# Optimization experiments

Measured on AMD Instinct MI355X. Metric: run time of the kernel, lower is better.

The kernel has to match this reference:

```python
import jax, jax.numpy as jnp
import numpy as np

CODEBOOK_SIZE = 1024
NUM_GROUPS = 8
CODES_PER_GROUP = CODEBOOK_SIZE // NUM_GROUPS
COMMITMENT_COST = 0.25


def setup_inputs() -> dict:
    key = jax.random.key(0)
    k1, k2, k3 = jax.random.split(key, 3)
    B, C, H, W = 32, 256, 32, 32
    z = jax.random.normal(k1, (B, C, H, W), dtype=jnp.float32)
    # matches nn.Embedding init: uniform(-1/n_e, 1/n_e)
    emb_weight = jax.random.uniform(
        k2, (CODEBOOK_SIZE, C), dtype=jnp.float32,
        minval=-1.0 / CODEBOOK_SIZE, maxval=1.0 / CODEBOOK_SIZE)
    # proj initialized near identity (nn.init.eye_), perturbed so it is non-trivial
    proj_weight = jnp.eye(C, dtype=jnp.float32) + 0.01 * jax.random.normal(
        k3, (C, C), dtype=jnp.float32)
    return {"z": z, "emb_weight": emb_weight, "proj_weight": proj_weight}


def reference(z, emb_weight, proj_weight):
    # z: [B, C, H, W] -> [B, H, W, C]
    B, C, H, W = z.shape
    zc = jnp.transpose(z, (0, 2, 3, 1))          # bhwc
    zf = zc.reshape(-1, C)                        # [N, C], N = B*H*W

    # codebook = embedding_proj(embedding.weight) = emb @ proj.T
    codebook = emb_weight @ proj_weight.T         # [n_e, C]

    # squared L2 distances: [N, n_e]
    d = (jnp.sum(zf * zf, axis=1, keepdims=True)
         + jnp.sum(codebook * codebook, axis=1)
         - 2.0 * (zf @ codebook.T))

    # group-restricted mask: token group depends on width position
    pos_groups = (jnp.arange(W) * NUM_GROUPS) // W          # [W]
    token_groups = jnp.tile(pos_groups, B * H)              # [N]
    code_groups = jnp.arange(CODEBOOK_SIZE) // CODES_PER_GROUP  # [n_e]
    valid = token_groups[:, None] == code_groups[None, :]   # [N, n_e]
    d = jnp.where(valid, d, jnp.inf)

    idx = jnp.argmin(d, axis=1)                   # [N]
    zq = codebook[idx].reshape(zc.shape)          # [B, H, W, C]

    commitment_loss = COMMITMENT_COST * jnp.mean(
        (jax.lax.stop_gradient(zq) - zc) ** 2)
    codebook_loss = jnp.mean((zq - jax.lax.stop_gradient(zc)) ** 2)
    loss = commitment_loss + codebook_loss

    # straight-through estimator
    zq_ste = zc + jax.lax.stop_gradient(zq - zc)
    zq_out = jnp.transpose(zq_ste, (0, 3, 1, 2))  # [B, C, H, W]

    return (zq_out, loss, commitment_loss, codebook_loss,
            idx.reshape(B, H, W))
```

## Files before the change

### kernel.cpp

```cpp
#include <hip/hip_runtime.h>

#define CODEBOOK 1024
#define NGROUPS  8
#define CPG      128
#define Bn 32
#define Cn 256
#define Hn 32
#define Wn 32

#define ZQ_OFF   0
#define LOSS_OFF (Bn*Cn*Hn*Wn)
#define IDX_OFF  (LOSS_OFF + 3)

__global__ __launch_bounds__(256) void transpose_proj(const float* __restrict__ proj,
                                                      float* __restrict__ projT,
                                                      double* __restrict__ lacc) {
    if (blockIdx.x == 0 && threadIdx.x == 0) lacc[0] = 0.0;
    int k = blockIdx.x;
    int j = threadIdx.x;
    projT[(size_t)k * Cn + j] = proj[(size_t)j * Cn + k];
}

__global__ __launch_bounds__(256) void codebook_kernel(const float* __restrict__ emb,
                                                       const float* __restrict__ projT,
                                                       float* __restrict__ cb) {
    __shared__ float emb8[8][Cn];
    const int t  = threadIdx.x;
    const int i0 = blockIdx.x * 8;
#pragma unroll
    for (int m = 0; m < 8; ++m) {
        int id = t + m * 256;
        int ci = id >> 8, k = id & 255;
        emb8[ci][k] = emb[(size_t)(i0 + ci) * Cn + k];
    }
    __syncthreads();
    float acc[8] = {0.f,0.f,0.f,0.f,0.f,0.f,0.f,0.f};
    for (int k = 0; k < Cn; ++k) {
        float pj = projT[(size_t)k * Cn + t];
#pragma unroll
        for (int ci = 0; ci < 8; ++ci)
            acc[ci] = __builtin_fmaf(emb8[ci][k], pj, acc[ci]);
    }
#pragma unroll
    for (int ci = 0; ci < 8; ++ci)
        cb[(size_t)(i0 + ci) * Cn + t] = acc[ci];
}

__global__ __launch_bounds__(64) void norm_kernel(const float* __restrict__ cb,
                                                  float* __restrict__ norms) {
    int i = blockIdx.x, l = threadIdx.x;
    float4 v = *(const float4*)(cb + (size_t)i * Cn + l * 4);
    float s = v.x*v.x + v.y*v.y + v.z*v.z + v.w*v.w;
#pragma unroll
    for (int off = 32; off > 0; off >>= 1) s += __shfl_down(s, off);
    if (l == 0) norms[i] = s;
}

__global__ __launch_bounds__(256) void vq_main(const float* __restrict__ z,
                                               const float* __restrict__ cb,
                                               const float* __restrict__ norms,
                                               float* __restrict__ out,
                                               double* __restrict__ lacc) {
    __shared__ float ztile[64][64];
    __shared__ float cbt[128][64];
    __shared__ float zfin[64];
    __shared__ float red_d[64][16];
    __shared__ int   red_c[64][16];
    __shared__ int   bestidx[64];

    const int t   = threadIdx.x;
    const int bid = blockIdx.x;
    const int r   = bid & 7;
    const int q   = bid >> 3;
    const int g   = q & 7;
    const int s   = ((q >> 3) << 3) | r;
    const int ht  = s & 1;
    const int b   = s >> 1;
    const int h0  = ht * 16;
    const int w0  = g * 4;

    const float* zb  = z  + (size_t)b * (Cn * Hn * Wn);
    const float* cbg = cb + (size_t)g * CPG * Cn;

    const int tok0  = (t & 15) * 4;
    const int code0 = (t >> 4) * 8;

    float acc[4][8];
#pragma unroll
    for (int rr2 = 0; rr2 < 4; ++rr2)
#pragma unroll
        for (int c = 0; c < 8; ++c) acc[rr2][c] = 0.f;

    float zr[16];
#pragma unroll
    for (int p = 0; p < 16; ++p) zr[p] = 0.f;

    for (int kc = 0; kc < 4; ++kc) {
        const int k0 = kc * 64;
#pragma unroll
        for (int m = 0; m < 4; ++m) {
            int id = t + m * 256;
            int kk = id >> 4, i = id & 15;
            float4 v = *(const float4*)(zb + (size_t)(k0 + kk) * (Hn * Wn)
                                        + (h0 + i) * Wn + w0);
            *(float4*)&ztile[kk][i * 4] = v;
        }
#pragma unroll
        for (int m = 0; m < 8; ++m) {
            int id = t + m * 256;
            int ci = id >> 4, kq = id & 15;
            float4 v = *(const float4*)(cbg + (size_t)ci * Cn + k0 + kq * 4);
            ((float4*)&cbt[ci][0])[kq ^ (ci >> 3)] = v;
        }
        __syncthreads();

        if (t < 64) {
#pragma clang fp contract(off)
            {
                const int base8 = (kc >> 1) * 8;
                for (int kk = 0; kk < 64; ++kk) {
                    float v  = ztile[kk][t];
                    float sq = v * v;
                    zr[base8 + (kk & 7)] += sq;
                }
            }
        }

        for (int kb = 0; kb < 16; ++kb) {
            const int kk = kb * 4;
            float4 zt[4];
#pragma unroll
            for (int u = 0; u < 4; ++u)
                zt[u] = *(const float4*)&ztile[kk + u][tok0];
            float4 cf[8];
#pragma unroll
            for (int c = 0; c < 8; ++c)
                cf[c] = ((const float4*)&cbt[code0 + c][0])[kb ^ ((code0 + c) >> 3)];
#pragma unroll
            for (int u = 0; u < 4; ++u) {
                const float zu[4] = {
                    zt[u].x, zt[u].y, zt[u].z, zt[u].w };
                const float cu[8] = {
                    ((const float*)&cf[0])[u], ((const float*)&cf[1])[u],
                    ((const float*)&cf[2])[u], ((const float*)&cf[3])[u],
                    ((const float*)&cf[4])[u], ((const float*)&cf[5])[u],
                    ((const float*)&cf[6])[u], ((const float*)&cf[7])[u] };
#pragma unroll
                for (int rr3 = 0; rr3 < 4; ++rr3)
#pragma unroll
                    for (int c = 0; c < 8; ++c)
                        acc[rr3][c] = __builtin_fmaf(zu[rr3], cu[c], acc[rr3][c]);
            }
        }
        __syncthreads();
    }

    if (t < 64) {
#pragma clang fp contract(off)
        {
            float zh0 = ((zr[0] + zr[1]) + (zr[2] + zr[3]))
                      + ((zr[4] + zr[5]) + (zr[6] + zr[7]));
            float zh1 = ((zr[8] + zr[9]) + (zr[10] + zr[11]))
                      + ((zr[12] + zr[13]) + (zr[14] + zr[15]));
            zfin[t] = zh0 + zh1;
        }
    }
    __syncthreads();

    float nv[8];
    *(float4*)&nv[0] = *(const float4*)(norms + g * CPG + code0);
    *(float4*)&nv[4] = *(const float4*)(norms + g * CPG + code0 + 4);
#pragma unroll
    for (int rr4 = 0; rr4 < 4; ++rr4) {
        float zv = zfin[tok0 + rr4];
        float bd = __builtin_inff();
        int   bc = 0;
#pragma unroll
        for (int c = 0; c < 8; ++c) {
            float ss = zv + nv[c];
            float d  = ss - 2.0f * acc[rr4][c];
            if (d < bd) { bd = d; bc = code0 + c; }
        }
        red_d[tok0 + rr4][t >> 4] = bd;
        red_c[tok0 + rr4][t >> 4] = bc;
    }
    __syncthreads();

    if (t < 64) {
        float bd = red_d[t][0];
        int   bc = red_c[t][0];
        for (int p = 1; p < 16; ++p) {
            float d = red_d[t][p];
            if (d < bd) { bd = d; bc = red_c[t][p]; }
        }
        int gidx = g * CPG + bc;
        bestidx[t] = gidx;
        int h = h0 + (t >> 2), w = w0 + (t & 3);
        out[IDX_OFF + b * (Hn * Wn) + h * Wn + w] = (float)gidx;
    }
    __syncthreads();

    float lsum = 0.f;
    const size_t zbase = (size_t)b * (Cn * Hn * Wn);
#pragma unroll
    for (int m = 0; m < 16; ++m) {
        int id = t + m * 256;
        int c = id >> 4, i = id & 15;
        size_t off = zbase + (size_t)c * (Hn * Wn) + (h0 + i) * Wn + w0;
        float4 zv = *(const float4*)(z + off);
        float q0 = cb[(size_t)bestidx[i * 4 + 0] * Cn + c];
        float q1 = cb[(size_t)bestidx[i * 4 + 1] * Cn + c];
        float q2 = cb[(size_t)bestidx[i * 4 + 2] * Cn + c];
        float q3 = cb[(size_t)bestidx[i * 4 + 3] * Cn + c];
        float4 o; o.x = q0; o.y = q1; o.z = q2; o.w = q3;
        *(float4*)(out + ZQ_OFF + off) = o;
        float d0 = q0 - zv.x, d1 = q1 - zv.y, d2 = q2 - zv.z, d3 = q3 - zv.w;
        lsum = __builtin_fmaf(d0, d0, lsum);
        lsum = __builtin_fmaf(d1, d1, lsum);
        lsum = __builtin_fmaf(d2, d2, lsum);
        lsum = __builtin_fmaf(d3, d3, lsum);
    }
    __syncthreads();
    float* rr = &red_d[0][0];
    rr[t] = lsum;
    __syncthreads();
    for (int s2 = 128; s2 > 0; s2 >>= 1) {
        if (t < s2) rr[t] += rr[t + s2];
        __syncthreads();
    }
    if (t == 0) atomicAdd(lacc, (double)rr[0]);
}

__global__ void finalize(const double* __restrict__ lacc, float* __restrict__ out) {
    float M    = (float)(lacc[0] / (double)(Bn * Cn * Hn * Wn));
    float comm = 0.25f * M;
    out[LOSS_OFF + 0] = comm + M;
    out[LOSS_OFF + 1] = comm;
    out[LOSS_OFF + 2] = M;
}

extern "C" void kernel_launch(void* const* d_in, const int* in_sizes, int n_in,
                              void* d_out, int out_size, void* d_ws, size_t ws_size,
                              hipStream_t stream) {
    (void)in_sizes; (void)n_in; (void)out_size; (void)ws_size;
    const float* z    = (const float*)d_in[0];
    const float* emb  = (const float*)d_in[1];
    const float* proj = (const float*)d_in[2];
    float* out = (float*)d_out;

    char*   ws    = (char*)d_ws;
    float*  projT = (float*)ws;
    float*  cb    = (float*)(ws + 262144);
    float*  norms = (float*)(ws + 262144 + 1048576);
    double* lacc  = (double*)(ws + 262144 + 1048576 + 4096);

    transpose_proj <<<Cn,        256, 0, stream>>>(proj, projT, lacc);
    codebook_kernel<<<CODEBOOK/8,256, 0, stream>>>(emb, projT, cb);
    norm_kernel    <<<CODEBOOK,   64, 0, stream>>>(cb, norms);
    vq_main        <<<Bn*2*NGROUPS,256,0, stream>>>(z, cb, norms, out, lacc);
    finalize       <<<1, 1, 0, stream>>>(lacc, out);
}
```

Measured before the change: 175.7 us.

## Fuse codebook, transpose and norm kernels; prefetch tiles; fold finalize into vq_main

```diff
diff --git a/kernel.cpp b/kernel.cpp
--- a/kernel.cpp
+++ b/kernel.cpp
@@ -12,55 +12,72 @@
 #define LOSS_OFF (Bn*Cn*Hn*Wn)
 #define IDX_OFF  (LOSS_OFF + 3)
 
-__global__ __launch_bounds__(256) void transpose_proj(const float* __restrict__ proj,
-                                                      float* __restrict__ projT,
-                                                      double* __restrict__ lacc) {
-    if (blockIdx.x == 0 && threadIdx.x == 0) lacc[0] = 0.0;
-    int k = blockIdx.x;
-    int j = threadIdx.x;
-    projT[(size_t)k * Cn + j] = proj[(size_t)j * Cn + k];
-}
-
-__global__ __launch_bounds__(256) void codebook_kernel(const float* __restrict__ emb,
-                                                       const float* __restrict__ projT,
-                                                       float* __restrict__ cb) {
-    __shared__ float emb8[8][Cn];
+#define KT 32
+__global__ __launch_bounds__(256) void codebook_fused(const float* __restrict__ emb,
+                                                      const float* __restrict__ proj,
+                                                      float* __restrict__ cb,
+                                                      float* __restrict__ norms,
+                                                      double* __restrict__ lacc,
+                                                      int* __restrict__ counter) {
+    __shared__ float emb4[4][Cn];
+    __shared__ float pl[KT][Cn + 1];
     const int t  = threadIdx.x;
-    const int i0 = blockIdx.x * 8;
-#pragma unroll
-    for (int m = 0; m < 8; ++m) {
+    const int i0 = blockIdx.x * 4;
+    if (blockIdx.x == 0 && t == 0) { lacc[0] = 0.0; counter[0] = 0; }
+#pragma unroll
+    for (int m = 0; m < 4; ++m) {
         int id = t + m * 256;
         int ci = id >> 8, k = id & 255;
-        emb8[ci][k] = emb[(size_t)(i0 + ci) * Cn + k];
-    }
-    __syncthreads();
-    float acc[8] = {0.f,0.f,0.f,0.f,0.f,0.f,0.f,0.f};
-    for (int k = 0; k < Cn; ++k) {
-        float pj = projT[(size_t)k * Cn + t];
-#pragma unroll
-        for (int ci = 0; ci < 8; ++ci)
-            acc[ci] = __builtin_fmaf(emb8[ci][k], pj, acc[ci]);
-    }
-#pragma unroll
-    for (int ci = 0; ci < 8; ++ci)
+        emb4[ci][k] = emb[(size_t)(i0 + ci) * Cn + k];
+    }
+    float acc[4] = {0.f, 0.f, 0.f, 0.f};
+    for (int kc = 0; kc < Cn / KT; ++kc) {
+        const int k0 = kc * KT;
+        __syncthreads();
+#pragma unroll
+        for (int m = 0; m < 8; ++m) {
+            int id  = t + m * 256;
+            int row = id >> 3, q = id & 7;
+            float4 v = *(const float4*)(proj + (size_t)row * Cn + k0 + q * 4);
+            pl[q * 4 + 0][row] = v.x;
+            pl[q * 4 + 1][row] = v.y;
+            pl[q * 4 + 2][row] = v.z;
+            pl[q * 4 + 3][row] = v.w;
+        }
+        __syncthreads();
+        for (int kl = 0; kl < KT; ++kl) {
+            float pj = pl[kl][t];
+#pragma unroll
+            for (int ci = 0; ci < 4; ++ci)
+                acc[ci] = __builtin_fmaf(emb4[ci][k0 + kl], pj, acc[ci]);
+        }
+    }
+    __syncthreads();
+    float (*cbrow)[Cn] = (float (*)[Cn])&pl[0][0];
+#pragma unroll
+    for (int ci = 0; ci < 4; ++ci) {
         cb[(size_t)(i0 + ci) * Cn + t] = acc[ci];
-}
-
-__global__ __launch_bounds__(64) void norm_kernel(const float* __restrict__ cb,
-                                                  float* __restrict__ norms) {
-    int i = blockIdx.x, l = threadIdx.x;
-    float4 v = *(const float4*)(cb + (size_t)i * Cn + l * 4);
-    float s = v.x*v.x + v.y*v.y + v.z*v.z + v.w*v.w;
-#pragma unroll
-    for (int off = 32; off > 0; off >>= 1) s += __shfl_down(s, off);
-    if (l == 0) norms[i] = s;
+        cbrow[ci][t] = acc[ci];
+    }
+    __syncthreads();
+    if (t < 64) {
+#pragma unroll
+        for (int ci = 0; ci < 4; ++ci) {
+            float4 v = ((const float4*)&cbrow[ci][0])[t];
+            float s = v.x*v.x + v.y*v.y + v.z*v.z + v.w*v.w;
+#pragma unroll
+            for (int off = 32; off > 0; off >>= 1) s += __shfl_down(s, off);
+            if (t == 0) norms[i0 + ci] = s;
+        }
+    }
 }
 
 __global__ __launch_bounds__(256) void vq_main(const float* __restrict__ z,
                                                const float* __restrict__ cb,
                                                const float* __restrict__ norms,
                                                float* __restrict__ out,
-                                               double* __restrict__ lacc) {
+                                               double* __restrict__ lacc,
+                                               int* __restrict__ counter) {
     __shared__ float ztile[64][64];
     __shared__ float cbt[128][64];
     __shared__ float zfin[64];
@@ -95,24 +112,35 @@
 #pragma unroll
     for (int p = 0; p < 16; ++p) zr[p] = 0.f;
 
+    int z_kk[4], z_i[4], c_ci[8], c_kq[8];
+#pragma unroll
+    for (int m = 0; m < 4; ++m) { int id = t + m * 256; z_kk[m] = id >> 4; z_i[m] = id & 15; }
+#pragma unroll
+    for (int m = 0; m < 8; ++m) { int id = t + m * 256; c_ci[m] = id >> 4; c_kq[m] = id & 15; }
+
+    float4 pz[4], pcb[8];
+    auto issue_loads = [&](int k0) {
+#pragma unroll
+        for (int m = 0; m < 4; ++m)
+            pz[m] = *(const float4*)(zb + (size_t)(k0 + z_kk[m]) * (Hn * Wn)
+                                     + (h0 + z_i[m]) * Wn + w0);
+#pragma unroll
+        for (int m = 0; m < 8; ++m)
+            pcb[m] = *(const float4*)(cbg + (size_t)c_ci[m] * Cn + k0 + c_kq[m] * 4);
+    };
+
+    issue_loads(0);
     for (int kc = 0; kc < 4; ++kc) {
         const int k0 = kc * 64;
-#pragma unroll
-        for (int m = 0; m < 4; ++m) {
-            int id = t + m * 256;
-            int kk = id >> 4, i = id & 15;
-            float4 v = *(const float4*)(zb + (size_t)(k0 + kk) * (Hn * Wn)
-                                        + (h0 + i) * Wn + w0);
-            *(float4*)&ztile[kk][i * 4] = v;
-        }
-#pragma unroll
-        for (int m = 0; m < 8; ++m) {
-            int id = t + m * 256;
-            int ci = id >> 4, kq = id & 15;
-            float4 v = *(const float4*)(cbg + (size_t)ci * Cn + k0 + kq * 4);
-            ((float4*)&cbt[ci][0])[kq ^ (ci >> 3)] = v;
-        }
-        __syncthreads();
+        if (kc) __syncthreads();
+#pragma unroll
+        for (int m = 0; m < 4; ++m)
+            *(float4*)&ztile[z_kk[m]][z_i[m] * 4] = pz[m];
+#pragma unroll
+        for (int m = 0; m < 8; ++m)
+            ((float4*)&cbt[c_ci[m]][0])[c_kq[m] ^ (c_ci[m] >> 3)] = pcb[m];
+        __syncthreads();
+        if (kc < 3) issue_loads(k0 + 64);
 
         if (t < 64) {
 #pragma clang fp contract(off)
@@ -152,7 +180,6 @@
                         acc[rr3][c] = __builtin_fmaf(zu[rr3], cu[c], acc[rr3][c]);
             }
         }
-        __syncthreads();
     }
 
     if (t < 64) {
@@ -228,15 +255,19 @@
         if (t < s2) rr[t] += rr[t + s2];
         __syncthreads();
     }
-    if (t == 0) atomicAdd(lacc, (double)rr[0]);
-}
-
-__global__ void finalize(const double* __restrict__ lacc, float* __restrict__ out) {
-    float M    = (float)(lacc[0] / (double)(Bn * Cn * Hn * Wn));
-    float comm = 0.25f * M;
-    out[LOSS_OFF + 0] = comm + M;
-    out[LOSS_OFF + 1] = comm;
-    out[LOSS_OFF + 2] = M;
+    if (t == 0) {
+        atomicAdd(lacc, (double)rr[0]);
+        __threadfence();
+        int done = atomicAdd(counter, 1);
+        if (done == (int)gridDim.x - 1) {
+            double tot = atomicAdd(lacc, 0.0);
+            float M    = (float)(tot / (double)(Bn * Cn * Hn * Wn));
+            float comm = 0.25f * M;
+            out[LOSS_OFF + 0] = comm + M;
+            out[LOSS_OFF + 1] = comm;
+            out[LOSS_OFF + 2] = M;
+        }
+    }
 }
 
 extern "C" void kernel_launch(void* const* d_in, const int* in_sizes, int n_in,
@@ -248,15 +279,12 @@
     const float* proj = (const float*)d_in[2];
     float* out = (float*)d_out;
 
-    char*   ws    = (char*)d_ws;
-    float*  projT = (float*)ws;
-    float*  cb    = (float*)(ws + 262144);
-    float*  norms = (float*)(ws + 262144 + 1048576);
-    double* lacc  = (double*)(ws + 262144 + 1048576 + 4096);
-
-    transpose_proj <<<Cn,        256, 0, stream>>>(proj, projT, lacc);
-    codebook_kernel<<<CODEBOOK/8,256, 0, stream>>>(emb, projT, cb);
-    norm_kernel    <<<CODEBOOK,   64, 0, stream>>>(cb, norms);
-    vq_main        <<<Bn*2*NGROUPS,256,0, stream>>>(z, cb, norms, out, lacc);
-    finalize       <<<1, 1, 0, stream>>>(lacc, out);
+    char*   ws      = (char*)d_ws;
+    float*  cb      = (float*)ws;
+    float*  norms   = (float*)(ws + 1048576);
+    double* lacc    = (double*)(ws + 1048576 + 4096);
+    int*    counter = (int*)(ws + 1048576 + 4096 + 8);
+
+    codebook_fused<<<CODEBOOK/4, 256, 0, stream>>>(emb, proj, cb, norms, lacc, counter);
+    vq_main       <<<Bn*2*NGROUPS, 256, 0, stream>>>(z, cb, norms, out, lacc, counter);
 }
```

Measured after the change: 237.7 us. +35.3%, slower.
